# Optimization experiments

Hardware: AMD Instinct MI355X
Metric: run time of the kernel (lower is better)

Reference implementation:

```python
import jax, jax.numpy as jnp
import numpy as np

B, T, D, H = 2, 2048, 2048, 16
HS = D // H  # head size 128


def setup_inputs() -> dict:
    key = jax.random.key(0)
    ks = jax.random.split(key, 5)
    s = 0.02
    return {
        "x": jax.random.normal(ks[0], (B, T, D), dtype=jnp.float32),
        "wq": jax.random.normal(ks[1], (D, D), dtype=jnp.float32) * s,
        "wk": jax.random.normal(ks[2], (D, D), dtype=jnp.float32) * s,
        "wv": jax.random.normal(ks[3], (D, D), dtype=jnp.float32) * s,
        "wo": jax.random.normal(ks[4], (D, D), dtype=jnp.float32) * s,
    }


def reference(x, wq, wk, wv, wo):
    b, t, d = x.shape
    # projections: nn.Linear(x) = x @ W.T ; here W stored as (out,in)
    q = (x @ wq.T).reshape(b, t, H, HS).transpose(0, 2, 1, 3)  # (B,H,T,HS)
    k = (x @ wk.T).reshape(b, t, H, HS).transpose(0, 2, 1, 3)
    v = (x @ wv.T).reshape(b, t, H, HS).transpose(0, 2, 1, 3)
    scale = 1.0 / np.sqrt(HS).astype(np.float32)
    e = jnp.einsum("bhqd,bhkd->bhqk", q, k) * scale  # (B,H,T,T)
    causal = jnp.tril(jnp.ones((t, t), dtype=bool))
    e = jnp.where(causal[None, None], e, jnp.float32(-jnp.inf))
    alpha = jax.nn.softmax(e, axis=-1)  # dropout=0.0 -> identity
    attn = jnp.einsum("bhqk,bhkd->bhqd", alpha, v)
    attn = attn.transpose(0, 2, 1, 3).reshape(b, t, d)
    return attn @ wo.T
```

## Files before the change

### kernel.cpp

```cpp
#include <hip/hip_runtime.h>
#include <hip/hip_bf16.h>

typedef __bf16 bf16x8 __attribute__((ext_vector_type(8)));
typedef float f32x4 __attribute__((ext_vector_type(4)));
typedef unsigned short u16x8 __attribute__((ext_vector_type(8)));

#define GLDS16(g, s)                                                         \
  __builtin_amdgcn_global_load_lds(                                          \
      (const __attribute__((address_space(1))) void*)(g),                    \
      (__attribute__((address_space(3))) void*)(s), 16, 0, 0)

__device__ __forceinline__ void store1(__hip_bfloat16* p, float v) { *p = __float2bfloat16(v); }
__device__ __forceinline__ void store1(float* p, float v) { *p = v; }

__global__ __launch_bounds__(256) void cast_f32_to_bf16(const float4* __restrict__ in,
                                                        ushort4* __restrict__ out, int n4) {
  int i = blockIdx.x * 256 + threadIdx.x;
  if (i >= n4) return;
  float4 v = in[i];
  union { ushort4 u; __hip_bfloat16 h[4]; } o;
  o.h[0] = __float2bfloat16(v.x);
  o.h[1] = __float2bfloat16(v.y);
  o.h[2] = __float2bfloat16(v.z);
  o.h[3] = __float2bfloat16(v.w);
  out[i] = o.u;
}

template <typename OutT>
__global__ __launch_bounds__(256) void gemm_bt(const __hip_bfloat16* __restrict__ A,
                                               const __hip_bfloat16* __restrict__ B,
                                               OutT* __restrict__ C,
                                               int M, int N, int K) {
  __shared__ __hip_bfloat16 As[128 * 32];
  __shared__ __hip_bfloat16 Bs[128 * 32];
  const int t = threadIdx.x;
  const int w = t >> 6, l = t & 63;
  const int m0 = blockIdx.y * 128;
  const int n0 = blockIdx.x * 128;
  const int wm = (w >> 1) * 64, wn = (w & 1) * 64;

  const int r0 = t >> 2, e0 = (t & 3) * 8;
  const __hip_bfloat16* a0 = A + (size_t)(m0 + r0) * K + e0;
  const __hip_bfloat16* a1 = A + (size_t)(m0 + r0 + 64) * K + e0;
  const __hip_bfloat16* b0 = B + (size_t)(n0 + r0) * K + e0;
  const __hip_bfloat16* b1 = B + (size_t)(n0 + r0 + 64) * K + e0;

  f32x4 acc[4][4] = {};
  const int lr = l & 15;
  const int lkB = (l >> 4) * 16;

  for (int k0 = 0; k0 < K; k0 += 32) {
    __syncthreads();
    GLDS16(a0 + k0, (char*)As + t * 16);
    GLDS16(a1 + k0, (char*)As + t * 16 + 4096);
    GLDS16(b0 + k0, (char*)Bs + t * 16);
    GLDS16(b1 + k0, (char*)Bs + t * 16 + 4096);
    __syncthreads();

    bf16x8 af[4], bfr[4];
#pragma unroll
    for (int mi = 0; mi < 4; ++mi)
      af[mi] = *(const bf16x8*)((const char*)As + (wm + mi * 16 + lr) * 64 + lkB);
#pragma unroll
    for (int ni = 0; ni < 4; ++ni)
      bfr[ni] = *(const bf16x8*)((const char*)Bs + (wn + ni * 16 + lr) * 64 + lkB);
#pragma unroll
    for (int mi = 0; mi < 4; ++mi)
#pragma unroll
      for (int ni = 0; ni < 4; ++ni)
        acc[mi][ni] = __builtin_amdgcn_mfma_f32_16x16x32_bf16(af[mi], bfr[ni], acc[mi][ni], 0, 0, 0);
  }

  const int crow = (l >> 4) * 4, ccol = l & 15;
#pragma unroll
  for (int mi = 0; mi < 4; ++mi)
#pragma unroll
    for (int ni = 0; ni < 4; ++ni)
#pragma unroll
      for (int i = 0; i < 4; ++i) {
        size_t idx = (size_t)(m0 + wm + mi * 16 + crow + i) * N + (n0 + wn + ni * 16 + ccol);
        store1(&C[idx], acc[mi][ni][i]);
      }
}

__global__ __launch_bounds__(256, 2) void flash_attn(const __hip_bfloat16* __restrict__ Qg,
                                                     const __hip_bfloat16* __restrict__ Kg,
                                                     const __hip_bfloat16* __restrict__ Vg,
                                                     __hip_bfloat16* __restrict__ Og) {
  __shared__ __hip_bfloat16 Ks[2][64 * 128];
  __shared__ __hip_bfloat16 Vt[128 * 64];

  const int mblk = blockIdx.x;
  const int bh = mblk & 31;
  const int jj = mblk >> 5;
  const int qt = (jj < 8) ? (15 - jj) : (jj - 8);
  const int b = bh >> 4, h = bh & 15;
  const int q0 = qt * 128;
  const int t = threadIdx.x, w = t >> 6, l = t & 63;
  const int lr = l & 15, hi = l >> 4;
  const size_t base = ((size_t)b * 2048) * 2048 + (size_t)h * 128;
  const int nt = 2 * qt + 2;
  const float scale = 0.08838834764831843f;

  const int hi2 = (hi & 1) * 2;
  const int addrA = (((hi2) << 4) | lr) << 2;
  const int addrB = (((hi2 + 1) << 4) | lr) << 2;
  int addr_o[4];
#pragma unroll
  for (int i = 0; i < 4; ++i) addr_o[i] = ((l & 48) | (hi * 4 + i)) << 2;
  const bool hiHigh = (hi >> 1) != 0;

  bf16x8 qf[2][4];
#pragma unroll
  for (int g = 0; g < 2; ++g) {
    const __hip_bfloat16* qrow = Qg + base + (size_t)(q0 + w * 32 + g * 16 + lr) * 2048;
#pragma unroll
    for (int kk = 0; kk < 4; ++kk)
      qf[g][kk] = *(const bf16x8*)(qrow + kk * 32 + hi * 8);
  }

  f32x4 o_acc[2][8] = {};
  float m_run[2] = {-1e30f, -1e30f};
  float l_run[2] = {0.f, 0.f};

  const __hip_bfloat16* kptr[4];
#pragma unroll
  for (int i = 0; i < 4; ++i) {
    int c = i * 256 + t;
    int kr = c >> 4;
    int ke = ((c & 15) ^ (kr & 7)) * 8;
    kptr[i] = Kg + base + (size_t)kr * 2048 + ke;
  }
  const __hip_bfloat16* vptr[2];
#pragma unroll
  for (int it = 0; it < 2; ++it) {
    int kp = it * 16 + w * 4 + hi;
    vptr[it] = Vg + base + (size_t)(kp * 2) * 2048 + lr * 8;
  }

  u16x8 va[2], vb[2];
#pragma unroll
  for (int i = 0; i < 4; ++i)
    GLDS16(kptr[i], (char*)Ks[0] + (i * 256 + t) * 16);
#pragma unroll
  for (int it = 0; it < 2; ++it) {
    va[it] = *(const u16x8*)vptr[it];
    vb[it] = *(const u16x8*)(vptr[it] + 2048);
  }

  for (int kt = 0; kt < nt; ++kt) {
    const int cur = kt & 1;
    const int kb = kt * 64;
    __syncthreads();

#pragma unroll
    for (int it = 0; it < 2; ++it)
#pragma unroll
      for (int j2 = 0; j2 < 8; ++j2) {
        int d = lr * 8 + j2;
        int sw = (lr ^ j2) & 7;
        int off = d * 128 + (((it * 4 + w) ^ sw) << 4) + hi * 4;
        *(unsigned int*)((char*)Vt + off) =
            (unsigned int)va[it][j2] | ((unsigned int)vb[it][j2] << 16);
      }
    if (kt + 1 < nt) {
      const size_t adv = (size_t)(kb + 64) * 2048;
#pragma unroll
      for (int i = 0; i < 4; ++i)
        GLDS16(kptr[i] + adv, (char*)Ks[cur ^ 1] + (i * 256 + t) * 16);
#pragma unroll
      for (int it = 0; it < 2; ++it) {
        va[it] = *(const u16x8*)(vptr[it] + adv);
        vb[it] = *(const u16x8*)(vptr[it] + adv + 2048);
      }
    }
    asm volatile("s_waitcnt lgkmcnt(0)" ::: "memory");
    __builtin_amdgcn_s_barrier();

    if (!(kt == nt - 1 && w < 2)) {
      const char* ks = (const char*)Ks[cur];

      f32x4 st[2][4];
#pragma unroll
      for (int g = 0; g < 2; ++g)
#pragma unroll
        for (int nk = 0; nk < 4; ++nk) { f32x4 z = {}; st[g][nk] = z; }
#pragma unroll
      for (int nk = 0; nk < 4; ++nk)
#pragma unroll
        for (int kk = 0; kk < 4; ++kk) {
          bf16x8 kf = *(const bf16x8*)(ks + (nk * 16 + lr) * 256 +
                                       (((kk * 4 + hi) ^ (lr & 7)) << 4));
#pragma unroll
          for (int g = 0; g < 2; ++g)
            st[g][nk] = __builtin_amdgcn_mfma_f32_16x16x32_bf16(kf, qf[g][kk], st[g][nk], 0, 0, 0);
        }

      const bool maskt = (kt >= nt - 2);
#pragma unroll
      for (int g = 0; g < 2; ++g)
#pragma unroll
        for (int nk = 0; nk < 4; ++nk)
#pragma unroll
          for (int i = 0; i < 4; ++i) {
            float v = st[g][nk][i] * scale;
            if (maskt) {
              int ki = kb + nk * 16 + hi * 4 + i;
              int qi = q0 + w * 32 + g * 16 + lr;
              if (ki > qi) v = -1e30f;
            }
            st[g][nk][i] = v;
          }

      bf16x8 paf[2][2];
#pragma unroll
      for (int g = 0; g < 2; ++g) {
        float t0 = fmaxf(fmaxf(st[g][0][0], st[g][0][1]), fmaxf(st[g][0][2], st[g][0][3]));
        float t1 = fmaxf(fmaxf(st[g][1][0], st[g][1][1]), fmaxf(st[g][1][2], st[g][1][3]));
        float t2 = fmaxf(fmaxf(st[g][2][0], st[g][2][1]), fmaxf(st[g][2][2], st[g][2][3]));
        float t3 = fmaxf(fmaxf(st[g][3][0], st[g][3][1]), fmaxf(st[g][3][2], st[g][3][3]));
        float mx = fmaxf(fmaxf(t0, t1), fmaxf(t2, t3));
        mx = fmaxf(mx, __shfl_xor(mx, 16));
        mx = fmaxf(mx, __shfl_xor(mx, 32));

        if (!__all(mx - m_run[g] <= 8.0f)) {
          float mnew = fmaxf(m_run[g], mx);
          float rs = __expf(m_run[g] - mnew);
          m_run[g] = mnew;
          l_run[g] *= rs;
          int rsi = __float_as_int(rs);
#pragma unroll
          for (int i = 0; i < 4; ++i) {
            float rso = __int_as_float(__builtin_amdgcn_ds_bpermute(addr_o[i], rsi));
#pragma unroll
            for (int nc = 0; nc < 8; ++nc) o_acc[g][nc][i] *= rso;
          }
        }

#pragma unroll
        for (int nk = 0; nk < 4; ++nk)
#pragma unroll
          for (int i = 0; i < 4; ++i)
            st[g][nk][i] = __expf(st[g][nk][i] - m_run[g]);

        float s0 = (st[g][0][0] + st[g][0][1]) + (st[g][0][2] + st[g][0][3]);
        float s1 = (st[g][1][0] + st[g][1][1]) + (st[g][1][2] + st[g][1][3]);
        float s2 = (st[g][2][0] + st[g][2][1]) + (st[g][2][2] + st[g][2][3]);
        float s3 = (st[g][3][0] + st[g][3][1]) + (st[g][3][2] + st[g][3][3]);
        float sm = (s0 + s1) + (s2 + s3);
        sm += __shfl_xor(sm, 16);
        sm += __shfl_xor(sm, 32);
        l_run[g] += sm;

        unsigned pk[4][2];
#pragma unroll
        for (int nk = 0; nk < 4; ++nk) {
          asm("v_cvt_pk_bf16_f32 %0, %1, %2"
              : "=v"(pk[nk][0]) : "v"(st[g][nk][0]), "v"(st[g][nk][1]));
          asm("v_cvt_pk_bf16_f32 %0, %1, %2"
              : "=v"(pk[nk][1]) : "v"(st[g][nk][2]), "v"(st[g][nk][3]));
        }

#pragma unroll
        for (int kk = 0; kk < 2; ++kk) {
          unsigned au[4];
#pragma unroll
          for (int p = 0; p < 4; ++p) {
            int ad = (p < 2) ? addrA : addrB;
            int v0 = __builtin_amdgcn_ds_bpermute(ad, (int)pk[2 * kk][p & 1]);
            int v1 = __builtin_amdgcn_ds_bpermute(ad, (int)pk[2 * kk + 1][p & 1]);
            au[p] = hiHigh ? (unsigned)v1 : (unsigned)v0;
          }
          union { unsigned u[4]; bf16x8 v; } cv;
          cv.u[0] = au[0]; cv.u[1] = au[1]; cv.u[2] = au[2]; cv.u[3] = au[3];
          paf[g][kk] = cv.v;
        }
      }

#pragma unroll
      for (int kk = 0; kk < 2; ++kk)
#pragma unroll
        for (int nc = 0; nc < 8; ++nc) {
          int d = nc * 16 + lr;
          int sw = ((d >> 3) ^ d) & 7;
          bf16x8 vfr = *(const bf16x8*)((const char*)Vt + d * 128 +
                                        (((kk * 4 + hi) ^ sw) << 4));
#pragma unroll
          for (int g = 0; g < 2; ++g)
            o_acc[g][nc] = __builtin_amdgcn_mfma_f32_16x16x32_bf16(paf[g][kk], vfr, o_acc[g][nc], 0, 0, 0);
        }
    }
  }

#pragma unroll
  for (int g = 0; g < 2; ++g) {
    float lo[4];
#pragma unroll
    for (int i = 0; i < 4; ++i)
      lo[i] = __int_as_float(__builtin_amdgcn_ds_bpermute(addr_o[i], __float_as_int(l_run[g])));
#pragma unroll
    for (int nc = 0; nc < 8; ++nc)
#pragma unroll
      for (int i = 0; i < 4; ++i) {
        float val = o_acc[g][nc][i] / lo[i];
        Og[base + (size_t)(q0 + w * 32 + g * 16 + hi * 4 + i) * 2048 + nc * 16 + lr] =
            __float2bfloat16(val);
      }
  }
}

extern "C" void kernel_launch(void* const* d_in, const int* in_sizes, int n_in,
                              void* d_out, int out_size, void* d_ws, size_t ws_size,
                              hipStream_t stream) {
  const float* x  = (const float*)d_in[0];
  const float* wq = (const float*)d_in[1];
  const float* wk = (const float*)d_in[2];
  const float* wv = (const float*)d_in[3];
  const float* wo = (const float*)d_in[4];
  float* out = (float*)d_out;

  const int BT = 4096, D = 2048;
  const size_t ND = (size_t)D * D;
  const size_t NX = (size_t)BT * D;

  __hip_bfloat16* xb  = (__hip_bfloat16*)d_ws;
  __hip_bfloat16* wqb = xb + NX;
  __hip_bfloat16* wkb = wqb + ND;
  __hip_bfloat16* wvb = wkb + ND;
  __hip_bfloat16* wob = wvb + ND;
  __hip_bfloat16* Qb  = wob + ND;
  __hip_bfloat16* Kb  = Qb + NX;
  __hip_bfloat16* Vb  = Kb + NX;
  __hip_bfloat16* Ab  = Vb + NX;

  cast_f32_to_bf16<<<(int)(NX / 4 / 256), 256, 0, stream>>>((const float4*)x,  (ushort4*)xb,  (int)(NX / 4));
  cast_f32_to_bf16<<<(int)(ND / 4 / 256), 256, 0, stream>>>((const float4*)wq, (ushort4*)wqb, (int)(ND / 4));
  cast_f32_to_bf16<<<(int)(ND / 4 / 256), 256, 0, stream>>>((const float4*)wk, (ushort4*)wkb, (int)(ND / 4));
  cast_f32_to_bf16<<<(int)(ND / 4 / 256), 256, 0, stream>>>((const float4*)wv, (ushort4*)wvb, (int)(ND / 4));
  cast_f32_to_bf16<<<(int)(ND / 4 / 256), 256, 0, stream>>>((const float4*)wo, (ushort4*)wob, (int)(ND / 4));

  dim3 gg(D / 128, BT / 128);
  gemm_bt<__hip_bfloat16><<<gg, 256, 0, stream>>>(xb, wqb, Qb, BT, D, D);
  gemm_bt<__hip_bfloat16><<<gg, 256, 0, stream>>>(xb, wkb, Kb, BT, D, D);
  gemm_bt<__hip_bfloat16><<<gg, 256, 0, stream>>>(xb, wvb, Vb, BT, D, D);

  flash_attn<<<512, 256, 0, stream>>>(Qb, Kb, Vb, Ab);

  gemm_bt<float><<<gg, 256, 0, stream>>>(Ab, wob, out, BT, D, D);
}
```

Before: 333.4 us.

## Replace GEMM with triple-buffered 256x128 swizzled kernel fusing QKV projections

Replaces the single-buffered 128x128 GEMM with a 512-thread, 256x128-tile kernel that uses a three-stage global-to-LDS pipeline with K-step 64, XOR-swizzled LDS layout, and s_setprio around MFMA bursts. The Q, K and V projections are merged into one launch that selects the weight and output per tile. A workgroup-id remap groups neighbouring tiles for cache locality. The aim is to hide load latency, cut per-iteration barrier overhead and LDS bank conflicts, and fill the GPU better, at the cost of more LDS per block (144KB), which may limit occupancy.

```diff
diff --git a/kernel.cpp b/kernel.cpp
--- a/kernel.cpp
+++ b/kernel.cpp
@@ -27,59 +27,117 @@
 }
 
 template <typename OutT>
-__global__ __launch_bounds__(256) void gemm_bt(const __hip_bfloat16* __restrict__ A,
-                                               const __hip_bfloat16* __restrict__ B,
-                                               OutT* __restrict__ C,
-                                               int M, int N, int K) {
-  __shared__ __hip_bfloat16 As[128 * 32];
-  __shared__ __hip_bfloat16 Bs[128 * 32];
+__global__ __launch_bounds__(512, 2) void gemm8p(const __hip_bfloat16* __restrict__ A,
+                                                 const __hip_bfloat16* __restrict__ B0,
+                                                 const __hip_bfloat16* __restrict__ B1,
+                                                 const __hip_bfloat16* __restrict__ B2,
+                                                 OutT* __restrict__ C0,
+                                                 OutT* __restrict__ C1,
+                                                 OutT* __restrict__ C2,
+                                                 int nBx, int nBy, int ntPerMat,
+                                                 int N, int K) {
+  __shared__ __hip_bfloat16 As[3][256 * 64];
+  __shared__ __hip_bfloat16 Bs[3][128 * 64];
+
   const int t = threadIdx.x;
   const int w = t >> 6, l = t & 63;
-  const int m0 = blockIdx.y * 128;
-  const int n0 = blockIdx.x * 128;
+  const int lr = l & 15, hi = l >> 4;
+
+  const int nwg = nBx * nBy;
+  int id = (int)blockIdx.x;
+  id = (id & 7) * (nwg >> 3) + (id >> 3);
+  const int bx = id % nBx;
+  const int by = id / nBx;
+
+  const int sel = bx / ntPerMat;
+  const __hip_bfloat16* Bm = (sel == 0) ? B0 : ((sel == 1) ? B1 : B2);
+  OutT* Cm = (sel == 0) ? C0 : ((sel == 1) ? C1 : C2);
+  const int n0 = (bx - sel * ntPerMat) * 128;
+  const int m0 = by * 256;
+
+  const __hip_bfloat16* aptr[4];
+#pragma unroll
+  for (int i = 0; i < 4; ++i) {
+    int c = i * 512 + t;
+    int row = c >> 3;
+    int slot = (c & 7) ^ (row & 7);
+    aptr[i] = A + (size_t)(m0 + row) * K + slot * 8;
+  }
+  const __hip_bfloat16* bptr[2];
+#pragma unroll
+  for (int i = 0; i < 2; ++i) {
+    int c = i * 512 + t;
+    int row = c >> 3;
+    int slot = (c & 7) ^ (row & 7);
+    bptr[i] = Bm + (size_t)(n0 + row) * K + slot * 8;
+  }
+
+#define STAGE_G(buf, tt)                                                     \
+  do {                                                                       \
+    const size_t koff = (size_t)(tt) * 64;                                   \
+    GLDS16(aptr[0] + koff, (char*)As[buf] + t * 16);                         \
+    GLDS16(aptr[1] + koff, (char*)As[buf] + t * 16 + 8192);                  \
+    GLDS16(aptr[2] + koff, (char*)As[buf] + t * 16 + 16384);                 \
+    GLDS16(aptr[3] + koff, (char*)As[buf] + t * 16 + 24576);                 \
+    GLDS16(bptr[0] + koff, (char*)Bs[buf] + t * 16);                         \
+    GLDS16(bptr[1] + koff, (char*)Bs[buf] + t * 16 + 8192);                  \
+  } while (0)
+
   const int wm = (w >> 1) * 64, wn = (w & 1) * 64;
-
-  const int r0 = t >> 2, e0 = (t & 3) * 8;
-  const __hip_bfloat16* a0 = A + (size_t)(m0 + r0) * K + e0;
-  const __hip_bfloat16* a1 = A + (size_t)(m0 + r0 + 64) * K + e0;
-  const __hip_bfloat16* b0 = B + (size_t)(n0 + r0) * K + e0;
-  const __hip_bfloat16* b1 = B + (size_t)(n0 + r0 + 64) * K + e0;
-
   f32x4 acc[4][4] = {};
-  const int lr = l & 15;
-  const int lkB = (l >> 4) * 16;
-
-  for (int k0 = 0; k0 < K; k0 += 32) {
-    __syncthreads();
-    GLDS16(a0 + k0, (char*)As + t * 16);
-    GLDS16(a1 + k0, (char*)As + t * 16 + 4096);
-    GLDS16(b0 + k0, (char*)Bs + t * 16);
-    GLDS16(b1 + k0, (char*)Bs + t * 16 + 4096);
-    __syncthreads();
-
-    bf16x8 af[4], bfr[4];
-#pragma unroll
-    for (int mi = 0; mi < 4; ++mi)
-      af[mi] = *(const bf16x8*)((const char*)As + (wm + mi * 16 + lr) * 64 + lkB);
+  const int NT = K / 64;
+  const int sw = lr & 7;
+
+  STAGE_G(0, 0);
+  STAGE_G(1, 1);
+  asm volatile("s_waitcnt vmcnt(6)" ::: "memory");
+  __builtin_amdgcn_s_barrier();
+
+  for (int tt = 0; tt < NT; ++tt) {
+    const int buf = tt % 3;
+    if (tt) {
+      if (tt + 1 < NT)
+        asm volatile("s_waitcnt vmcnt(6)" ::: "memory");
+      else
+        asm volatile("s_waitcnt vmcnt(0)" ::: "memory");
+      __builtin_amdgcn_s_barrier();
+    }
+    if (tt + 2 < NT) STAGE_G((tt + 2) % 3, tt + 2);
+
+    const char* as_ = (const char*)As[buf];
+    const char* bs_ = (const char*)Bs[buf];
+
+    bf16x8 bfr[4][2];
 #pragma unroll
     for (int ni = 0; ni < 4; ++ni)
-      bfr[ni] = *(const bf16x8*)((const char*)Bs + (wn + ni * 16 + lr) * 64 + lkB);
-#pragma unroll
-    for (int mi = 0; mi < 4; ++mi)
-#pragma unroll
-      for (int ni = 0; ni < 4; ++ni)
-        acc[mi][ni] = __builtin_amdgcn_mfma_f32_16x16x32_bf16(af[mi], bfr[ni], acc[mi][ni], 0, 0, 0);
-  }
-
-  const int crow = (l >> 4) * 4, ccol = l & 15;
+#pragma unroll
+      for (int kk = 0; kk < 2; ++kk)
+        bfr[ni][kk] = *(const bf16x8*)(bs_ + (wn + ni * 16 + lr) * 128 +
+                                       (((kk * 4 + hi) ^ sw) << 4));
+#pragma unroll
+    for (int mi = 0; mi < 4; ++mi) {
+      const char* arow = as_ + (wm + mi * 16 + lr) * 128;
+      bf16x8 a0 = *(const bf16x8*)(arow + ((hi ^ sw) << 4));
+      bf16x8 a1 = *(const bf16x8*)(arow + (((4 + hi) ^ sw) << 4));
+      __builtin_amdgcn_s_setprio(1);
+#pragma unroll
+      for (int ni = 0; ni < 4; ++ni) {
+        acc[mi][ni] = __builtin_amdgcn_mfma_f32_16x16x32_bf16(a0, bfr[ni][0], acc[mi][ni], 0, 0, 0);
+        acc[mi][ni] = __builtin_amdgcn_mfma_f32_16x16x32_bf16(a1, bfr[ni][1], acc[mi][ni], 0, 0, 0);
+      }
+      __builtin_amdgcn_s_setprio(0);
+    }
+  }
+#undef STAGE_G
+
 #pragma unroll
   for (int mi = 0; mi < 4; ++mi)
 #pragma unroll
     for (int ni = 0; ni < 4; ++ni)
 #pragma unroll
       for (int i = 0; i < 4; ++i) {
-        size_t idx = (size_t)(m0 + wm + mi * 16 + crow + i) * N + (n0 + wn + ni * 16 + ccol);
-        store1(&C[idx], acc[mi][ni][i]);
+        size_t idx = (size_t)(m0 + wm + mi * 16 + hi * 4 + i) * N + (n0 + wn + ni * 16 + lr);
+        store1(&Cm[idx], acc[mi][ni][i]);
       }
 }
 
@@ -339,12 +397,11 @@
   cast_f32_to_bf16<<<(int)(ND / 4 / 256), 256, 0, stream>>>((const float4*)wv, (ushort4*)wvb, (int)(ND / 4));
   cast_f32_to_bf16<<<(int)(ND / 4 / 256), 256, 0, stream>>>((const float4*)wo, (ushort4*)wob, (int)(ND / 4));
 
-  dim3 gg(D / 128, BT / 128);
-  gemm_bt<__hip_bfloat16><<<gg, 256, 0, stream>>>(xb, wqb, Qb, BT, D, D);
-  gemm_bt<__hip_bfloat16><<<gg, 256, 0, stream>>>(xb, wkb, Kb, BT, D, D);
-  gemm_bt<__hip_bfloat16><<<gg, 256, 0, stream>>>(xb, wvb, Vb, BT, D, D);
+  gemm8p<__hip_bfloat16><<<768, 512, 0, stream>>>(xb, wqb, wkb, wvb, Qb, Kb, Vb,
+                                                  48, 16, 16, D, D);
 
   flash_attn<<<512, 256, 0, stream>>>(Qb, Kb, Vb, Ab);
 
-  gemm_bt<float><<<gg, 256, 0, stream>>>(Ab, wob, out, BT, D, D);
+  gemm8p<float><<<256, 512, 0, stream>>>(Ab, wob, wob, wob, out, out, out,
+                                         16, 16, 16, D, D);
 }
```

New measurement: 302.4 us. -9.3%, faster.

## Replace 128x128 GEMM with pipelined 256x256 tile kernel and fuse QKV launches

Applied to the files above, without the earlier changes.

Replaces the simple single-buffered 128x128 bf16 GEMM with a 512-thread 256x256-tile kernel. It double-buffers 64-wide K slices in LDS using XOR-swizzled layout, issues next-tile loads in four phases interleaved with MFMA work, and raises wave priority during the math. The three Q/K/V projections become one launch that selects weight and output by tile column, and a grid remap groups workgroups for cache locality. This targets low arithmetic intensity, LDS bank conflicts and load/compute serialization. The cost is heavy register and LDS use (128KB LDS) and fewer workgroups for the output projection (128 blocks).

```diff
diff --git a/kernel.cpp b/kernel.cpp
--- a/kernel.cpp
+++ b/kernel.cpp
@@ -27,60 +27,121 @@
 }
 
 template <typename OutT>
-__global__ __launch_bounds__(256) void gemm_bt(const __hip_bfloat16* __restrict__ A,
-                                               const __hip_bfloat16* __restrict__ B,
-                                               OutT* __restrict__ C,
-                                               int M, int N, int K) {
-  __shared__ __hip_bfloat16 As[128 * 32];
-  __shared__ __hip_bfloat16 Bs[128 * 32];
+__global__ __launch_bounds__(512, 2) void gemm256(const __hip_bfloat16* __restrict__ A,
+                                                  const __hip_bfloat16* __restrict__ B0,
+                                                  const __hip_bfloat16* __restrict__ B1,
+                                                  const __hip_bfloat16* __restrict__ B2,
+                                                  OutT* __restrict__ C0,
+                                                  OutT* __restrict__ C1,
+                                                  OutT* __restrict__ C2,
+                                                  int nBx, int nBy, int ntPerMat,
+                                                  int N, int K) {
+  __shared__ __hip_bfloat16 As[2][256 * 64];
+  __shared__ __hip_bfloat16 Bs[2][256 * 64];
+
   const int t = threadIdx.x;
   const int w = t >> 6, l = t & 63;
-  const int m0 = blockIdx.y * 128;
-  const int n0 = blockIdx.x * 128;
-  const int wm = (w >> 1) * 64, wn = (w & 1) * 64;
-
-  const int r0 = t >> 2, e0 = (t & 3) * 8;
-  const __hip_bfloat16* a0 = A + (size_t)(m0 + r0) * K + e0;
-  const __hip_bfloat16* a1 = A + (size_t)(m0 + r0 + 64) * K + e0;
-  const __hip_bfloat16* b0 = B + (size_t)(n0 + r0) * K + e0;
-  const __hip_bfloat16* b1 = B + (size_t)(n0 + r0 + 64) * K + e0;
-
-  f32x4 acc[4][4] = {};
-  const int lr = l & 15;
-  const int lkB = (l >> 4) * 16;
-
-  for (int k0 = 0; k0 < K; k0 += 32) {
-    __syncthreads();
-    GLDS16(a0 + k0, (char*)As + t * 16);
-    GLDS16(a1 + k0, (char*)As + t * 16 + 4096);
-    GLDS16(b0 + k0, (char*)Bs + t * 16);
-    GLDS16(b1 + k0, (char*)Bs + t * 16 + 4096);
-    __syncthreads();
-
-    bf16x8 af[4], bfr[4];
-#pragma unroll
-    for (int mi = 0; mi < 4; ++mi)
-      af[mi] = *(const bf16x8*)((const char*)As + (wm + mi * 16 + lr) * 64 + lkB);
-#pragma unroll
-    for (int ni = 0; ni < 4; ++ni)
-      bfr[ni] = *(const bf16x8*)((const char*)Bs + (wn + ni * 16 + lr) * 64 + lkB);
-#pragma unroll
-    for (int mi = 0; mi < 4; ++mi)
-#pragma unroll
-      for (int ni = 0; ni < 4; ++ni)
-        acc[mi][ni] = __builtin_amdgcn_mfma_f32_16x16x32_bf16(af[mi], bfr[ni], acc[mi][ni], 0, 0, 0);
-  }
-
-  const int crow = (l >> 4) * 4, ccol = l & 15;
-#pragma unroll
-  for (int mi = 0; mi < 4; ++mi)
-#pragma unroll
-    for (int ni = 0; ni < 4; ++ni)
-#pragma unroll
-      for (int i = 0; i < 4; ++i) {
-        size_t idx = (size_t)(m0 + wm + mi * 16 + crow + i) * N + (n0 + wn + ni * 16 + ccol);
-        store1(&C[idx], acc[mi][ni][i]);
-      }
+  const int lr = l & 15, hi = l >> 4;
+
+  const int nwg = nBx * nBy;
+  int id = (int)blockIdx.x;
+  id = (id & 7) * (nwg >> 3) + (id >> 3);
+  const int bx = id % nBx;
+  const int by = id / nBx;
+
+  const int sel = bx / ntPerMat;
+  const __hip_bfloat16* Bm = (sel == 0) ? B0 : ((sel == 1) ? B1 : B2);
+  OutT* Cm = (sel == 0) ? C0 : ((sel == 1) ? C1 : C2);
+  const int n0 = (bx - sel * ntPerMat) * 256;
+  const int m0 = by * 256;
+
+  const int c0r = t >> 3, cs = t & 7;
+  const int c1r = 64 + c0r;
+  const __hip_bfloat16* aP0 = A + (size_t)(m0 + c0r) * K + (cs ^ (c0r & 7)) * 8;
+  const __hip_bfloat16* aP1 = A + (size_t)(m0 + c1r) * K + (cs ^ (c1r & 7)) * 8;
+  const __hip_bfloat16* bP0 = Bm + (size_t)(n0 + c0r) * K + (cs ^ (c0r & 7)) * 8;
+  const __hip_bfloat16* bP1 = Bm + (size_t)(n0 + c1r) * K + (cs ^ (c1r & 7)) * 8;
+  const size_t HK = (size_t)128 * K;
+
+#define STAGE_S(sidx, nb, koff)                                              \
+  do {                                                                       \
+    if ((sidx) == 0) {                                                       \
+      GLDS16(aP0 + (koff), (char*)As[nb] + t * 16);                          \
+      GLDS16(aP1 + (koff), (char*)As[nb] + 8192 + t * 16);                   \
+    } else if ((sidx) == 1) {                                                \
+      GLDS16(bP0 + (koff), (char*)Bs[nb] + t * 16);                          \
+      GLDS16(bP1 + (koff), (char*)Bs[nb] + 8192 + t * 16);                   \
+    } else if ((sidx) == 2) {                                                \
+      GLDS16(aP0 + HK + (koff), (char*)As[nb] + 16384 + t * 16);             \
+      GLDS16(aP1 + HK + (koff), (char*)As[nb] + 24576 + t * 16);             \
+    } else {                                                                 \
+      GLDS16(bP0 + HK + (koff), (char*)Bs[nb] + 16384 + t * 16);             \
+      GLDS16(bP1 + HK + (koff), (char*)Bs[nb] + 24576 + t * 16);             \
+    }                                                                        \
+  } while (0)
+
+  f32x4 acc[2][2][4][2] = {};
+  const int NT = K / 64;
+  const int sw = lr & 7;
+
+#define PHASE(mh, nh, sidx)                                                  \
+  do {                                                                       \
+    asm volatile("s_waitcnt vmcnt(4)" ::: "memory");                         \
+    __builtin_amdgcn_s_barrier();                                            \
+    const char* as_ = (const char*)As[buf];                                  \
+    const char* bs_ = (const char*)Bs[buf];                                  \
+    bf16x8 af[4][2], bq[2][2];                                               \
+    _Pragma("unroll") for (int mi = 0; mi < 4; ++mi)                         \
+      _Pragma("unroll") for (int kk = 0; kk < 2; ++kk)                       \
+        af[mi][kk] = *(const bf16x8*)(as_ +                                  \
+            ((mh) * 128 + (w >> 2) * 64 + mi * 16 + lr) * 128 +              \
+            (((kk * 4 + hi) ^ sw) << 4));                                    \
+    _Pragma("unroll") for (int ni = 0; ni < 2; ++ni)                         \
+      _Pragma("unroll") for (int kk = 0; kk < 2; ++kk)                       \
+        bq[ni][kk] = *(const bf16x8*)(bs_ +                                  \
+            ((nh) * 128 + (w & 3) * 32 + ni * 16 + lr) * 128 +               \
+            (((kk * 4 + hi) ^ sw) << 4));                                    \
+    if (tt + 1 < NT) STAGE_S((sidx), nb, (size_t)(tt + 1) * 64);             \
+    __builtin_amdgcn_s_setprio(1);                                           \
+    _Pragma("unroll") for (int mi = 0; mi < 4; ++mi)                         \
+      _Pragma("unroll") for (int ni = 0; ni < 2; ++ni) {                     \
+        acc[mh][nh][mi][ni] = __builtin_amdgcn_mfma_f32_16x16x32_bf16(       \
+            af[mi][0], bq[ni][0], acc[mh][nh][mi][ni], 0, 0, 0);             \
+        acc[mh][nh][mi][ni] = __builtin_amdgcn_mfma_f32_16x16x32_bf16(       \
+            af[mi][1], bq[ni][1], acc[mh][nh][mi][ni], 0, 0, 0);             \
+      }                                                                      \
+    __builtin_amdgcn_s_setprio(0);                                           \
+  } while (0)
+
+  STAGE_S(0, 0, 0);
+  STAGE_S(1, 0, 0);
+  STAGE_S(2, 0, 0);
+  STAGE_S(3, 0, 0);
+
+  for (int tt = 0; tt < NT; ++tt) {
+    const int buf = tt & 1, nb = buf ^ 1;
+    PHASE(0, 0, 0);
+    PHASE(1, 0, 1);
+    PHASE(0, 1, 2);
+    PHASE(1, 1, 3);
+  }
+#undef PHASE
+#undef STAGE_S
+
+#pragma unroll
+  for (int mh = 0; mh < 2; ++mh)
+#pragma unroll
+    for (int nh = 0; nh < 2; ++nh)
+#pragma unroll
+      for (int mi = 0; mi < 4; ++mi)
+#pragma unroll
+        for (int ni = 0; ni < 2; ++ni)
+#pragma unroll
+          for (int i = 0; i < 4; ++i) {
+            size_t idx = (size_t)(m0 + mh * 128 + (w >> 2) * 64 + mi * 16 + hi * 4 + i) * N +
+                         (n0 + nh * 128 + (w & 3) * 32 + ni * 16 + lr);
+            store1(&Cm[idx], acc[mh][nh][mi][ni][i]);
+          }
 }
 
 __global__ __launch_bounds__(256, 2) void flash_attn(const __hip_bfloat16* __restrict__ Qg,
@@ -339,12 +400,11 @@
   cast_f32_to_bf16<<<(int)(ND / 4 / 256), 256, 0, stream>>>((const float4*)wv, (ushort4*)wvb, (int)(ND / 4));
   cast_f32_to_bf16<<<(int)(ND / 4 / 256), 256, 0, stream>>>((const float4*)wo, (ushort4*)wob, (int)(ND / 4));
 
-  dim3 gg(D / 128, BT / 128);
-  gemm_bt<__hip_bfloat16><<<gg, 256, 0, stream>>>(xb, wqb, Qb, BT, D, D);
-  gemm_bt<__hip_bfloat16><<<gg, 256, 0, stream>>>(xb, wkb, Kb, BT, D, D);
-  gemm_bt<__hip_bfloat16><<<gg, 256, 0, stream>>>(xb, wvb, Vb, BT, D, D);
+  gemm256<__hip_bfloat16><<<384, 512, 0, stream>>>(xb, wqb, wkb, wvb, Qb, Kb, Vb,
+                                                   24, 16, 8, D, D);
 
   flash_attn<<<512, 256, 0, stream>>>(Qb, Kb, Vb, Ab);
 
-  gemm_bt<float><<<gg, 256, 0, stream>>>(Ab, wob, out, BT, D, D);
+  gemm256<float><<<128, 512, 0, stream>>>(Ab, wob, wob, wob, out, out, out,
+                                          8, 16, 8, D, D);
 }
```

Measured after the change: 302.0 us. 1.1x faster.
